# Performance work log

Measured on AMD Instinct MI355X. Metric: run time of the kernel, lower is better.

## Reference

```python
import jax, jax.numpy as jnp
import numpy as np

NUM_USERS = 50000
NUM_ITEMS = 50000
N_NODES = NUM_USERS + NUM_ITEMS
DIM_FEAT = 256
HID = 128
EMB = 128
K = 3
N_EDGES = 1_600_000


def setup_inputs() -> dict:
    key = jax.random.key(0)
    ks = jax.random.split(key, 16)

    def xavier(k, shape):
        fan_in, fan_out = shape[-2], shape[-1]
        std = float(np.sqrt(2.0 / (fan_in + fan_out)))
        return jax.random.normal(k, shape, dtype=jnp.float32) * std

    return {
        "feat": jax.random.normal(ks[0], (NUM_ITEMS, DIM_FEAT), dtype=jnp.float32),
        "node_emb": jax.random.normal(ks[1], (N_NODES, EMB), dtype=jnp.float32),
        "src": jax.random.randint(ks[2], (N_EDGES,), 0, N_NODES, dtype=jnp.int32),
        "dst": jax.random.randint(ks[3], (N_EDGES,), 0, N_NODES, dtype=jnp.int32),
        "user_feat_emb": xavier(ks[4], (NUM_USERS, HID)),
        "trans_w": xavier(ks[5], (DIM_FEAT, HID)),
        "trans_b": jnp.zeros((HID,), dtype=jnp.float32),
        # layer 0: hidden->hidden; layers 1,2: emb->emb. hidden==emb so stack.
        "ws": xavier(ks[6], (K, HID, HID)),
        "des_w": xavier(ks[7], (K, HID, EMB)),
        "des_b": jnp.zeros((K, EMB), dtype=jnp.float32),
        # concat=True: outs[i] takes [h | u] of width hidden+emb
        "out_w": xavier(ks[8], (K, HID + EMB, EMB)),
        "out_b": jnp.zeros((K, EMB), dtype=jnp.float32),
    }


def reference(feat, node_emb, src, dst, user_feat_emb,
              trans_w, trans_b, ws, des_w, des_b, out_w, out_b):
    # feat = trans(feat); concat user embeddings; L2-normalize rows
    x = feat @ trans_w + trans_b                      # [num_items, HID]
    x = jnp.concatenate([user_feat_emb, x], axis=0)   # [N, HID]
    norm = jnp.linalg.norm(x, axis=1, keepdims=True)
    x = x / jnp.maximum(norm, 1e-12)

    lrelu = jax.nn.leaky_relu  # slope 0.01, matches F.leaky_relu default
    for i in range(K):
        # g.func(x, W): sparse adjacency aggregation (sum over in-edges) then dense W
        agg = jax.ops.segment_sum(x[src], dst, num_segments=N_NODES)  # [N, HID]
        h = lrelu(agg @ ws[i])                                        # [N, HID]
        u = lrelu(h @ des_w[i] + des_b[i] + node_emb)                 # [N, EMB]
        x = lrelu(jnp.concatenate([h, u], axis=1) @ out_w[i] + out_b[i])
    return x, user_feat_emb
```

## Files before the change

kernel.cpp:

```cpp
#include <hip/hip_runtime.h>

#define NN 100000
#define NU 50000
#define NI 50000
#define NE 1600000
#define NSLICE 3
#define SLICEW 33334

#define HSLICE 4
#define HCHUNK 64
#define HSW 25600
#define HEPC (NE/HCHUNK)

typedef unsigned short u16;
typedef unsigned int u32;

typedef __attribute__((ext_vector_type(8))) short s16x8;
typedef __attribute__((ext_vector_type(4))) float f32x4;
typedef __attribute__((ext_vector_type(4))) unsigned short us4;

__device__ __forceinline__ float bf2f(u16 u){
  union { u32 i; float f; } v; v.i = ((u32)u) << 16; return v.f;
}
__device__ __forceinline__ u16 f2bf(float f){
  union { float f; u32 i; } v; v.f = f;
  u32 u = v.i;
  return (u16)((u + 0x7FFFu + ((u >> 16) & 1u)) >> 16);
}
__device__ __forceinline__ u32 pack2(float lo, float hi){
  return (u32)f2bf(lo) | ((u32)f2bf(hi) << 16);
}
__device__ __forceinline__ float lrelu(float x){ return x > 0.f ? x : 0.01f * x; }
__device__ __forceinline__ float san(float v){
  union { float f; u32 i; } u; u.f = v;
  return ((u.i & 0x7F800000u) == 0x7F800000u) ? 0.f : v;
}

__global__ __launch_bounds__(256) void transpose_weights(
    const float* __restrict__ trans_w, const float* __restrict__ wsw,
    const float* __restrict__ desw, const float* __restrict__ outw,
    u16* __restrict__ Ttw, u16* __restrict__ Tw, u16* __restrict__ Td, u16* __restrict__ To)
{
  __shared__ u16 L[128][136];
  int b = blockIdx.x, t = threadIdx.x;
  const float* src; u16* dst; int stride;
  if (b < 2)      { src = trans_w + b*16384;        dst = Ttw + b*128;          stride = 256; }
  else if (b < 5) { int i = b-2; src = wsw  + i*16384; dst = Tw + i*16384;      stride = 128; }
  else if (b < 8) { int i = b-5; src = desw + i*16384; dst = Td + i*16384;      stride = 128; }
  else            { int i = (b-8)>>1, h = (b-8)&1;
                    src = outw + i*32768 + h*16384;    dst = To + i*32768 + h*128; stride = 256; }
  #pragma unroll
  for (int p = 0; p < 8; p++){
    int fi = (p*256 + t)*8;
    int r = fi >> 7, c = fi & 127;
    f32x4 v0 = *(const f32x4*)(src + r*128 + c);
    f32x4 v1 = *(const f32x4*)(src + r*128 + c + 4);
    L[c+0][r] = f2bf(san(v0.x)); L[c+1][r] = f2bf(san(v0.y));
    L[c+2][r] = f2bf(san(v0.z)); L[c+3][r] = f2bf(san(v0.w));
    L[c+4][r] = f2bf(san(v1.x)); L[c+5][r] = f2bf(san(v1.y));
    L[c+6][r] = f2bf(san(v1.z)); L[c+7][r] = f2bf(san(v1.w));
  }
  __syncthreads();
  #pragma unroll
  for (int p = 0; p < 8; p++){
    int fi = (p*256 + t)*8;
    int n = fi >> 7, k = fi & 127;
    us4 o0, o1;
    o0.x = L[n][k+0]; o0.y = L[n][k+1]; o0.z = L[n][k+2]; o0.w = L[n][k+3];
    o1.x = L[n][k+4]; o1.y = L[n][k+5]; o1.z = L[n][k+6]; o1.w = L[n][k+7];
    *(us4*)(dst + (size_t)n*stride + k)     = o0;
    *(us4*)(dst + (size_t)n*stride + k + 4) = o1;
  }
}

__global__ __launch_bounds__(256) void conv_nemb(
    const float* __restrict__ nemb, u16* __restrict__ nembB)
{
  int i = blockIdx.x*256 + threadIdx.x;
  size_t off = (size_t)i * 8;
  f32x4 v0 = *(const f32x4*)(nemb + off);
  f32x4 v1 = *(const f32x4*)(nemb + off + 4);
  us4 o0, o1;
  o0.x = f2bf(san(v0.x)); o0.y = f2bf(san(v0.y)); o0.z = f2bf(san(v0.z)); o0.w = f2bf(san(v0.w));
  o1.x = f2bf(san(v1.x)); o1.y = f2bf(san(v1.y)); o1.z = f2bf(san(v1.z)); o1.w = f2bf(san(v1.w));
  *(us4*)(nembB + off)     = o0;
  *(us4*)(nembB + off + 4) = o1;
}

__global__ __launch_bounds__(256) void norm_users(const float* __restrict__ ufe, u16* __restrict__ X)
{
  int gid = blockIdx.x*256 + threadIdx.x;
  int row = gid >> 6, lane = gid & 63;
  float2 v = *(const float2*)(ufe + (size_t)row*128 + lane*2);
  float a = san(v.x), b = san(v.y);
  float ss = a*a + b*b;
  #pragma unroll
  for (int off = 32; off; off >>= 1) ss += __shfl_xor(ss, off, 64);
  float inv = 1.0f / fmaxf(sqrtf(ss), 1e-12f);
  *(u32*)(X + (size_t)row*128 + lane*2) = pack2(a*inv, b*inv);
}

__global__ __launch_bounds__(256, 4) void trans_items(
    const float* __restrict__ feat, const u16* __restrict__ Ttw,
    const float* __restrict__ tb, u16* __restrict__ X)
{
  __shared__ u16 Af[64][136];
  __shared__ float rowss[64][8];
  __shared__ float rnorm[64];

  int t = threadIdx.x;
  int r0 = blockIdx.x * 64;
  int w = t >> 6, lane = t & 63;
  int l15 = lane & 15, q = lane >> 4;
  int m0 = (w & 1) * 64, n0 = (w >> 1) * 32;

  f32x4 acc[4][2];
  #pragma unroll
  for (int mi = 0; mi < 4; mi++)
    #pragma unroll
    for (int ni = 0; ni < 2; ni++){ acc[mi][ni].x = 0.f; acc[mi][ni].y = 0.f; acc[mi][ni].z = 0.f; acc[mi][ni].w = 0.f; }

  for (int half = 0; half < 2; half++){
    __syncthreads();
    #pragma unroll
    for (int p = 0; p < 4; p++){
      int fi = (p*256 + t)*8;
      int r = fi >> 7, c = fi & 127;
      int row = r0 + r;
      us4 o0 = {0,0,0,0}, o1 = {0,0,0,0};
      if (row < NI){
        f32x4 v0 = *(const f32x4*)(feat + (size_t)row*256 + half*128 + c);
        f32x4 v1 = *(const f32x4*)(feat + (size_t)row*256 + half*128 + c + 4);
        o0.x = f2bf(san(v0.x)); o0.y = f2bf(san(v0.y)); o0.z = f2bf(san(v0.z)); o0.w = f2bf(san(v0.w));
        o1.x = f2bf(san(v1.x)); o1.y = f2bf(san(v1.y)); o1.z = f2bf(san(v1.z)); o1.w = f2bf(san(v1.w));
      }
      *(us4*)&Af[r][c]     = o0;
      *(us4*)&Af[r][c + 4] = o1;
    }
    __syncthreads();
    #pragma unroll
    for (int kc = 0; kc < 128; kc += 32){
      s16x8 afr[4], bfr[2];
      #pragma unroll
      for (int mi = 0; mi < 4; mi++)
        afr[mi] = *(const s16x8*)(Ttw + (size_t)(m0 + 16*mi + l15)*256 + half*128 + kc + 8*q);
      #pragma unroll
      for (int ni = 0; ni < 2; ni++) bfr[ni] = *(const s16x8*)&Af[n0 + 16*ni + l15][kc + 8*q];
      #pragma unroll
      for (int mi = 0; mi < 4; mi++)
        #pragma unroll
        for (int ni = 0; ni < 2; ni++)
          acc[mi][ni] = __builtin_amdgcn_mfma_f32_16x16x32_bf16(afr[mi], bfr[ni], acc[mi][ni], 0, 0, 0);
    }
  }

  float bias[4][4];
  #pragma unroll
  for (int mi = 0; mi < 4; mi++){
    int c0 = m0 + 16*mi + 4*q;
    f32x4 bv = *(const f32x4*)(tb + c0);
    bias[mi][0] = san(bv.x); bias[mi][1] = san(bv.y); bias[mi][2] = san(bv.z); bias[mi][3] = san(bv.w);
  }
  #pragma unroll
  for (int ni = 0; ni < 2; ni++){
    float ss = 0.f;
    #pragma unroll
    for (int mi = 0; mi < 4; mi++){
      float v0 = acc[mi][ni].x + bias[mi][0];
      float v1 = acc[mi][ni].y + bias[mi][1];
      float v2 = acc[mi][ni].z + bias[mi][2];
      float v3 = acc[mi][ni].w + bias[mi][3];
      ss += v0*v0 + v1*v1 + v2*v2 + v3*v3;
    }
    rowss[n0 + 16*ni + l15][(w & 1)*4 + q] = ss;
  }
  __syncthreads();
  if (t < 64){
    float s = 0.f;
    #pragma unroll
    for (int j = 0; j < 8; j++) s += rowss[t][j];
    rnorm[t] = 1.0f / fmaxf(sqrtf(s), 1e-12f);
  }
  __syncthreads();
  #pragma unroll
  for (int mi = 0; mi < 4; mi++){
    int c0 = m0 + 16*mi + 4*q;
    #pragma unroll
    for (int ni = 0; ni < 2; ni++){
      int r = n0 + 16*ni + l15;
      int row = r0 + r;
      if (row < NI){
        float inv = rnorm[r];
        us4 o;
        o.x = f2bf((acc[mi][ni].x + bias[mi][0]) * inv);
        o.y = f2bf((acc[mi][ni].y + bias[mi][1]) * inv);
        o.z = f2bf((acc[mi][ni].z + bias[mi][2]) * inv);
        o.w = f2bf((acc[mi][ni].w + bias[mi][3]) * inv);
        *(us4*)(X + (size_t)(NU + row)*128 + c0) = o;
      }
    }
  }
}

__global__ __launch_bounds__(1024) void hist_lds(
    const int* __restrict__ dst, u32* __restrict__ countsC)
{
  __shared__ u32 cnt[HSW];
  int b = blockIdx.x;
  int s = b / HCHUNK, c = b % HCHUNK;
  int t = threadIdx.x;
  for (int i = t; i < HSW; i += 1024) cnt[i] = 0;
  __syncthreads();
  int lo = s * HSW;
  int hi = min(lo + HSW, NN);
  int e0 = c * HEPC, e1 = e0 + HEPC;
  for (int e = e0 + t*4; e < e1; e += 4096){
    int4 d4 = *(const int4*)(dst + e);
    int d0 = min(max(d4.x, 0), NN-1);
    int d1 = min(max(d4.y, 0), NN-1);
    int d2 = min(max(d4.z, 0), NN-1);
    int d3 = min(max(d4.w, 0), NN-1);
    if (d0 >= lo && d0 < hi) atomicAdd(&cnt[d0 - lo], 1u);
    if (d1 >= lo && d1 < hi) atomicAdd(&cnt[d1 - lo], 1u);
    if (d2 >= lo && d2 < hi) atomicAdd(&cnt[d2 - lo], 1u);
    if (d3 >= lo && d3 < hi) atomicAdd(&cnt[d3 - lo], 1u);
  }
  __syncthreads();
  u32* outp = countsC + (size_t)c*NN + lo;
  int w = hi - lo;
  for (int i = t; i < w; i += 1024) outp[i] = cnt[i];
}

__global__ __launch_bounds__(256) void reduce_counts(
    const u32* __restrict__ countsC, int* __restrict__ counts)
{
  int v = blockIdx.x*256 + threadIdx.x;
  if (v < NN){
    u32 sum = 0;
    #pragma unroll
    for (int c = 0; c < HCHUNK; c++) sum += countsC[(size_t)c*NN + v];
    counts[v] = (int)sum;
  }
}

__global__ __launch_bounds__(1024) void scan_k(const int* __restrict__ counts, int* __restrict__ row_ptr){
  __shared__ int wsum[16];
  __shared__ int woff[16];
  __shared__ int tot;
  int t = threadIdx.x;
  int lane = t & 63, wid = t >> 6;
  int carry = 0;
  for (int base = 0; base < NN; base += 4096){
    int idx = base + t*4;
    int4 v = {0,0,0,0};
    if (idx < NN) v = *(const int4*)(counts + idx);
    int s4 = v.x + v.y + v.z + v.w;
    int s = s4;
    #pragma unroll
    for (int off = 1; off < 64; off <<= 1){
      int u = __shfl_up(s, off, 64);
      if (lane >= off) s += u;
    }
    if (lane == 63) wsum[wid] = s;
    __syncthreads();
    if (t < 16){
      int ws = wsum[t];
      int wscan = ws;
      #pragma unroll
      for (int off = 1; off < 16; off <<= 1){
        int u = __shfl_up(wscan, off, 64);
        if (t >= off) wscan += u;
      }
      woff[t] = wscan - ws;
      if (t == 15) tot = wscan;
    }
    __syncthreads();
    if (idx < NN){
      int e0 = carry + woff[wid] + (s - s4);
      int4 o;
      o.x = e0; o.y = e0 + v.x; o.z = o.y + v.y; o.w = o.z + v.z;
      *(int4*)(row_ptr + idx) = o;
    }
    carry += tot;
    __syncthreads();
  }
}

__global__ __launch_bounds__(256) void fill_slice(
    const int* __restrict__ src, const int* __restrict__ dst,
    int* __restrict__ row_ptr, int* __restrict__ esrc, int d0, int d1)
{
  int e = blockIdx.x*256 + threadIdx.x;
  if (e < NE){
    int d = dst[e];
    if (d >= d0 && d < d1){
      d = min(max(d, 0), NN - 1);
      int pos = atomicAdd(&row_ptr[d], 1);
      pos = min(max(pos, 0), NE - 1);
      esrc[pos] = src[e];
    }
  }
}

#define ACC8(P) \
  a0 += bf2f((u16)(P.x & 0xFFFF)); a1 += bf2f((u16)(P.x >> 16)); \
  a2 += bf2f((u16)(P.y & 0xFFFF)); a3 += bf2f((u16)(P.y >> 16)); \
  a4 += bf2f((u16)(P.z & 0xFFFF)); a5 += bf2f((u16)(P.z >> 16)); \
  a6 += bf2f((u16)(P.w & 0xFFFF)); a7 += bf2f((u16)(P.w >> 16));

__global__ __launch_bounds__(256) void aggregate(
    const u16* __restrict__ X, const int* __restrict__ row_ptr,
    const int* __restrict__ esrc, u16* __restrict__ AGG)
{
  int gid = blockIdx.x*256 + threadIdx.x;
  int v = gid >> 6, lane = gid & 63;
  int sub = lane >> 4, li = lane & 15;
  int jb = (v == 0) ? 0 : row_ptr[v - 1];
  int je = row_ptr[v];
  jb = min(max(jb, 0), NE);
  je = min(max(je, jb), NE);

  float a0=0.f,a1=0.f,a2=0.f,a3=0.f,a4=0.f,a5=0.f,a6=0.f,a7=0.f;

  int j = jb + sub;
  for (; j + 12 < je; j += 16){
    int s0 = esrc[j];      s0 = min(max(s0, 0), NN - 1);
    int s1 = esrc[j + 4];  s1 = min(max(s1, 0), NN - 1);
    int s2 = esrc[j + 8];  s2 = min(max(s2, 0), NN - 1);
    int s3 = esrc[j + 12]; s3 = min(max(s3, 0), NN - 1);
    uint4 p0 = *(const uint4*)(X + (size_t)s0*128 + li*8);
    uint4 p1 = *(const uint4*)(X + (size_t)s1*128 + li*8);
    uint4 p2 = *(const uint4*)(X + (size_t)s2*128 + li*8);
    uint4 p3 = *(const uint4*)(X + (size_t)s3*128 + li*8);
    ACC8(p0); ACC8(p1); ACC8(p2); ACC8(p3);
  }
  for (; j + 4 < je; j += 8){
    int s0 = esrc[j];     s0 = min(max(s0, 0), NN - 1);
    int s1 = esrc[j + 4]; s1 = min(max(s1, 0), NN - 1);
    uint4 p0 = *(const uint4*)(X + (size_t)s0*128 + li*8);
    uint4 p1 = *(const uint4*)(X + (size_t)s1*128 + li*8);
    ACC8(p0); ACC8(p1);
  }
  for (; j < je; j += 4){
    int s0 = esrc[j]; s0 = min(max(s0, 0), NN - 1);
    uint4 p0 = *(const uint4*)(X + (size_t)s0*128 + li*8);
    ACC8(p0);
  }

  a0 += __shfl_xor(a0, 16, 64); a0 += __shfl_xor(a0, 32, 64);
  a1 += __shfl_xor(a1, 16, 64); a1 += __shfl_xor(a1, 32, 64);
  a2 += __shfl_xor(a2, 16, 64); a2 += __shfl_xor(a2, 32, 64);
  a3 += __shfl_xor(a3, 16, 64); a3 += __shfl_xor(a3, 32, 64);
  a4 += __shfl_xor(a4, 16, 64); a4 += __shfl_xor(a4, 32, 64);
  a5 += __shfl_xor(a5, 16, 64); a5 += __shfl_xor(a5, 32, 64);
  a6 += __shfl_xor(a6, 16, 64); a6 += __shfl_xor(a6, 32, 64);
  a7 += __shfl_xor(a7, 16, 64); a7 += __shfl_xor(a7, 32, 64);

  if (sub == 0){
    uint4 o;
    o.x = pack2(a0, a1); o.y = pack2(a2, a3);
    o.z = pack2(a4, a5); o.w = pack2(a6, a7);
    *(uint4*)(AGG + (size_t)v*128 + li*8) = o;
  }
}

__global__ __launch_bounds__(256, 2) void layer_fused(
    const u16* __restrict__ AGG, const u16* __restrict__ nembB,
    const u16* __restrict__ Twi, const u16* __restrict__ Tdi,
    const float* __restrict__ dbF, const u16* __restrict__ Toi,
    const float* __restrict__ obF, u16* __restrict__ XoutB,
    float* __restrict__ XoutF, int last)
{
  __shared__ __align__(16) u16 Ab[128][136];
  __shared__ __align__(16) u16 Hb[128][136];

  int t = threadIdx.x;
  int r0 = blockIdx.x * 128;
  int w = t >> 6, lane = t & 63;
  int l15 = lane & 15, q = lane >> 4;
  int m0 = (w & 1) * 64, n0 = (w >> 1) * 64;

  f32x4 acc[4][4];

#define ZERO_ACC() \
  { _Pragma("unroll") for (int mi = 0; mi < 4; mi++) \
      { _Pragma("unroll") for (int ni = 0; ni < 4; ni++) \
        { acc[mi][ni].x = 0.f; acc[mi][ni].y = 0.f; acc[mi][ni].z = 0.f; acc[mi][ni].w = 0.f; } } }

#define GEMMG(BARR, WBASE, WSTRIDE, WKOFF) \
  { s16x8 afr[4][4]; \
    _Pragma("unroll") for (int mi = 0; mi < 4; mi++) \
      { _Pragma("unroll") for (int kk = 0; kk < 4; kk++) \
          afr[mi][kk] = *(const s16x8*)((WBASE) + (size_t)(m0 + 16*mi + l15)*(WSTRIDE) + (WKOFF) + kk*32 + 8*q); } \
    _Pragma("unroll") for (int kk = 0; kk < 4; kk++){ \
      s16x8 bfr[4]; \
      _Pragma("unroll") for (int ni = 0; ni < 4; ni++) bfr[ni] = *(const s16x8*)&BARR[n0 + 16*ni + l15][kk*32 + 8*q]; \
      _Pragma("unroll") for (int mi = 0; mi < 4; mi++) \
        { _Pragma("unroll") for (int ni = 0; ni < 4; ni++) \
          acc[mi][ni] = __builtin_amdgcn_mfma_f32_16x16x32_bf16(afr[mi][kk], bfr[ni], acc[mi][ni], 0, 0, 0); } } }

  #pragma unroll
  for (int p = 0; p < 8; p++){
    int fi = (p*256 + t)*8;
    int r = fi >> 7, c = fi & 127;
    int row = r0 + r;
    us4 o0 = {0,0,0,0}, o1 = {0,0,0,0};
    if (row < NN){
      o0 = *(const us4*)(AGG + (size_t)row*128 + c);
      o1 = *(const us4*)(AGG + (size_t)row*128 + c + 4);
    }
    *(us4*)&Ab[r][c]     = o0;
    *(us4*)&Ab[r][c + 4] = o1;
  }
  __syncthreads();

  ZERO_ACC();
  GEMMG(Ab, Twi, 128, 0);

  #pragma unroll
  for (int mi = 0; mi < 4; mi++){
    #pragma unroll
    for (int ni = 0; ni < 4; ni++){
      us4 o;
      o.x = f2bf(lrelu(acc[mi][ni].x));
      o.y = f2bf(lrelu(acc[mi][ni].y));
      o.z = f2bf(lrelu(acc[mi][ni].z));
      o.w = f2bf(lrelu(acc[mi][ni].w));
      *(us4*)&Hb[n0 + 16*ni + l15][m0 + 16*mi + 4*q] = o;
    }
  }
  __syncthreads();

  ZERO_ACC();
  GEMMG(Hb, Tdi, 128, 0);

  #pragma unroll
  for (int mi = 0; mi < 4; mi++){
    int c0 = m0 + 16*mi + 4*q;
    f32x4 dbv = *(const f32x4*)(dbF + c0);
    float db0 = san(dbv.x), db1 = san(dbv.y), db2 = san(dbv.z), db3 = san(dbv.w);
    #pragma unroll
    for (int ni = 0; ni < 4; ni++){
      int r = n0 + 16*ni + l15;
      int row = r0 + r;
      float e0 = 0.f, e1 = 0.f, e2 = 0.f, e3 = 0.f;
      if (row < NN){
        us4 ne = *(const us4*)(nembB + (size_t)row*128 + c0);
        e0 = bf2f(ne.x); e1 = bf2f(ne.y); e2 = bf2f(ne.z); e3 = bf2f(ne.w);
      }
      us4 o;
      o.x = f2bf(lrelu(acc[mi][ni].x + db0 + e0));
      o.y = f2bf(lrelu(acc[mi][ni].y + db1 + e1));
      o.z = f2bf(lrelu(acc[mi][ni].z + db2 + e2));
      o.w = f2bf(lrelu(acc[mi][ni].w + db3 + e3));
      *(us4*)&Ab[r][c0] = o;
    }
  }
  __syncthreads();

  ZERO_ACC();
  GEMMG(Hb, Toi, 256, 0);
  GEMMG(Ab, Toi, 256, 128);

  #pragma unroll
  for (int mi = 0; mi < 4; mi++){
    int c0 = m0 + 16*mi + 4*q;
    f32x4 obv = *(const f32x4*)(obF + c0);
    float b0 = san(obv.x), b1 = san(obv.y), b2 = san(obv.z), b3 = san(obv.w);
    #pragma unroll
    for (int ni = 0; ni < 4; ni++){
      int r = n0 + 16*ni + l15;
      int row = r0 + r;
      if (row < NN){
        if (last){
          f32x4 o;
          o.x = lrelu(acc[mi][ni].x + b0);
          o.y = lrelu(acc[mi][ni].y + b1);
          o.z = lrelu(acc[mi][ni].z + b2);
          o.w = lrelu(acc[mi][ni].w + b3);
          *(f32x4*)(XoutF + (size_t)row*128 + c0) = o;
        } else {
          us4 o;
          o.x = f2bf(lrelu(acc[mi][ni].x + b0));
          o.y = f2bf(lrelu(acc[mi][ni].y + b1));
          o.z = f2bf(lrelu(acc[mi][ni].z + b2));
          o.w = f2bf(lrelu(acc[mi][ni].w + b3));
          *(us4*)(XoutB + (size_t)row*128 + c0) = o;
        }
      }
    }
  }
#undef ZERO_ACC
#undef GEMMG
}

__global__ void copy_ufe(const float4* __restrict__ s, float4* __restrict__ d, int n){
  int i = blockIdx.x*256 + threadIdx.x;
  if (i < n){
    float4 v = s[i];
    v.x = san(v.x); v.y = san(v.y); v.z = san(v.z); v.w = san(v.w);
    d[i] = v;
  }
}

extern "C" void kernel_launch(void* const* d_in, const int* in_sizes, int n_in,
                              void* d_out, int out_size, void* d_ws, size_t ws_size,
                              hipStream_t stream)
{
  const float* feat = (const float*)d_in[0];
  const float* nemb = (const float*)d_in[1];
  const int*   src  = (const int*)d_in[2];
  const int*   dst  = (const int*)d_in[3];
  const float* ufe  = (const float*)d_in[4];
  const float* tw   = (const float*)d_in[5];
  const float* tb   = (const float*)d_in[6];
  const float* wsw  = (const float*)d_in[7];
  const float* desw = (const float*)d_in[8];
  const float* desb = (const float*)d_in[9];
  const float* outw = (const float*)d_in[10];
  const float* outb = (const float*)d_in[11];

  float* out  = (float*)d_out;
  float* outU = out + (size_t)NN*128;

  u16* X = (u16*)out;
  u16* nembB = (u16*)outU;

  char* p = (char*)d_ws;
  u16*   AGG = (u16*)p;    p += (size_t)NN*128*2;
  u16*   Ttw = (u16*)p;    p += (size_t)2*16384*2;
  u16*   Tw  = (u16*)p;    p += (size_t)3*16384*2;
  u16*   Td  = (u16*)p;    p += (size_t)3*16384*2;
  u16*   To  = (u16*)p;    p += (size_t)3*32768*2;
  int* row_ptr = (int*)p;  p += (size_t)100004*4;
  int* counts  = (int*)p;  p += (size_t)100000*4;
  int* esrc    = (int*)p;  p += (size_t)NE*4;
  u32* countsC = (u32*)AGG;

  transpose_weights<<<14, 256, 0, stream>>>(tw, wsw, desw, outw, Ttw, Tw, Td, To);
  conv_nemb<<<6250, 256, 0, stream>>>(nemb, nembB);
  norm_users<<<NU/4, 256, 0, stream>>>(ufe, X);
  trans_items<<<(NI + 63)/64, 256, 0, stream>>>(feat, Ttw, tb, X);

  hist_lds<<<HSLICE*HCHUNK, 1024, 0, stream>>>(dst, countsC);
  reduce_counts<<<(NN + 255)/256, 256, 0, stream>>>(countsC, counts);
  scan_k<<<1, 1024, 0, stream>>>(counts, row_ptr);
  for (int s = 0; s < NSLICE; s++){
    fill_slice<<<(NE + 255)/256, 256, 0, stream>>>(src, dst, row_ptr, esrc,
        s*SLICEW, (s == NSLICE-1) ? NN : (s+1)*SLICEW);
  }

  for (int i = 0; i < 3; i++){
    aggregate<<<NN/4, 256, 0, stream>>>(X, row_ptr, esrc, AGG);
    layer_fused<<<(NN + 127)/128, 256, 0, stream>>>(AGG, nembB,
        Tw + (size_t)i*16384, Td + (size_t)i*16384, desb + (size_t)i*128,
        To + (size_t)i*32768, outb + (size_t)i*128, X, out, (i == 2) ? 1 : 0);
  }
  copy_ufe<<<(NU*128/4 + 255)/256, 256, 0, stream>>>((const float4*)ufe, (float4*)outU, NU*128/4);
}
```

Measured before the change: 710.4 us.

## Merge prep kernels, parallelize prefix scan across blocks, use fewer fill slices

Three preprocessing kernels (weight transpose, node-embedding conversion, user normalization) are merged into one launch selected by block index. The single-block serial prefix scan over 100k counts becomes a three-phase multi-block scan using block sums. The fill pass is cut from three dst slices to two, so the edge arrays are read fewer times, but each slice now has more atomic targets and weaker locality. Together these aim to cut launch overhead and the serial scan latency.

```diff
diff --git a/kernel.cpp b/kernel.cpp
--- a/kernel.cpp
+++ b/kernel.cpp
@@ -4,14 +4,18 @@
 #define NU 50000
 #define NI 50000
 #define NE 1600000
-#define NSLICE 3
-#define SLICEW 33334
+#define NSLICE 2
+#define SLICEW 50000
 
 #define HSLICE 4
 #define HCHUNK 64
 #define HSW 25600
 #define HEPC (NE/HCHUNK)
 
+#define PREP_TW 14
+#define PREP_CONV 6250
+#define PREP_NORM 12500
+
 typedef unsigned short u16;
 typedef unsigned int u32;
 
@@ -36,68 +40,66 @@
   return ((u.i & 0x7F800000u) == 0x7F800000u) ? 0.f : v;
 }
 
-__global__ __launch_bounds__(256) void transpose_weights(
+__global__ __launch_bounds__(256) void prep(
     const float* __restrict__ trans_w, const float* __restrict__ wsw,
     const float* __restrict__ desw, const float* __restrict__ outw,
-    u16* __restrict__ Ttw, u16* __restrict__ Tw, u16* __restrict__ Td, u16* __restrict__ To)
+    u16* __restrict__ Ttw, u16* __restrict__ Tw, u16* __restrict__ Td, u16* __restrict__ To,
+    const float* __restrict__ nemb, u16* __restrict__ nembB,
+    const float* __restrict__ ufe, u16* __restrict__ X)
 {
   __shared__ u16 L[128][136];
   int b = blockIdx.x, t = threadIdx.x;
-  const float* src; u16* dst; int stride;
-  if (b < 2)      { src = trans_w + b*16384;        dst = Ttw + b*128;          stride = 256; }
-  else if (b < 5) { int i = b-2; src = wsw  + i*16384; dst = Tw + i*16384;      stride = 128; }
-  else if (b < 8) { int i = b-5; src = desw + i*16384; dst = Td + i*16384;      stride = 128; }
-  else            { int i = (b-8)>>1, h = (b-8)&1;
-                    src = outw + i*32768 + h*16384;    dst = To + i*32768 + h*128; stride = 256; }
-  #pragma unroll
-  for (int p = 0; p < 8; p++){
-    int fi = (p*256 + t)*8;
-    int r = fi >> 7, c = fi & 127;
-    f32x4 v0 = *(const f32x4*)(src + r*128 + c);
-    f32x4 v1 = *(const f32x4*)(src + r*128 + c + 4);
-    L[c+0][r] = f2bf(san(v0.x)); L[c+1][r] = f2bf(san(v0.y));
-    L[c+2][r] = f2bf(san(v0.z)); L[c+3][r] = f2bf(san(v0.w));
-    L[c+4][r] = f2bf(san(v1.x)); L[c+5][r] = f2bf(san(v1.y));
-    L[c+6][r] = f2bf(san(v1.z)); L[c+7][r] = f2bf(san(v1.w));
-  }
-  __syncthreads();
-  #pragma unroll
-  for (int p = 0; p < 8; p++){
-    int fi = (p*256 + t)*8;
-    int n = fi >> 7, k = fi & 127;
+
+  if (b < PREP_TW){
+    const float* src; u16* dst; int stride;
+    if (b < 2)      { src = trans_w + b*16384;        dst = Ttw + b*128;          stride = 256; }
+    else if (b < 5) { int i = b-2; src = wsw  + i*16384; dst = Tw + i*16384;      stride = 128; }
+    else if (b < 8) { int i = b-5; src = desw + i*16384; dst = Td + i*16384;      stride = 128; }
+    else            { int i = (b-8)>>1, h = (b-8)&1;
+                      src = outw + i*32768 + h*16384;    dst = To + i*32768 + h*128; stride = 256; }
+    #pragma unroll
+    for (int p = 0; p < 8; p++){
+      int fi = (p*256 + t)*8;
+      int r = fi >> 7, c = fi & 127;
+      f32x4 v0 = *(const f32x4*)(src + r*128 + c);
+      f32x4 v1 = *(const f32x4*)(src + r*128 + c + 4);
+      L[c+0][r] = f2bf(san(v0.x)); L[c+1][r] = f2bf(san(v0.y));
+      L[c+2][r] = f2bf(san(v0.z)); L[c+3][r] = f2bf(san(v0.w));
+      L[c+4][r] = f2bf(san(v1.x)); L[c+5][r] = f2bf(san(v1.y));
+      L[c+6][r] = f2bf(san(v1.z)); L[c+7][r] = f2bf(san(v1.w));
+    }
+    __syncthreads();
+    #pragma unroll
+    for (int p = 0; p < 8; p++){
+      int fi = (p*256 + t)*8;
+      int n = fi >> 7, k = fi & 127;
+      us4 o0, o1;
+      o0.x = L[n][k+0]; o0.y = L[n][k+1]; o0.z = L[n][k+2]; o0.w = L[n][k+3];
+      o1.x = L[n][k+4]; o1.y = L[n][k+5]; o1.z = L[n][k+6]; o1.w = L[n][k+7];
+      *(us4*)(dst + (size_t)n*stride + k)     = o0;
+      *(us4*)(dst + (size_t)n*stride + k + 4) = o1;
+    }
+  } else if (b < PREP_TW + PREP_CONV){
+    int i = (b - PREP_TW)*256 + t;
+    size_t off = (size_t)i * 8;
+    f32x4 v0 = *(const f32x4*)(nemb + off);
+    f32x4 v1 = *(const f32x4*)(nemb + off + 4);
     us4 o0, o1;
-    o0.x = L[n][k+0]; o0.y = L[n][k+1]; o0.z = L[n][k+2]; o0.w = L[n][k+3];
-    o1.x = L[n][k+4]; o1.y = L[n][k+5]; o1.z = L[n][k+6]; o1.w = L[n][k+7];
-    *(us4*)(dst + (size_t)n*stride + k)     = o0;
-    *(us4*)(dst + (size_t)n*stride + k + 4) = o1;
-  }
-}
-
-__global__ __launch_bounds__(256) void conv_nemb(
-    const float* __restrict__ nemb, u16* __restrict__ nembB)
-{
-  int i = blockIdx.x*256 + threadIdx.x;
-  size_t off = (size_t)i * 8;
-  f32x4 v0 = *(const f32x4*)(nemb + off);
-  f32x4 v1 = *(const f32x4*)(nemb + off + 4);
-  us4 o0, o1;
-  o0.x = f2bf(san(v0.x)); o0.y = f2bf(san(v0.y)); o0.z = f2bf(san(v0.z)); o0.w = f2bf(san(v0.w));
-  o1.x = f2bf(san(v1.x)); o1.y = f2bf(san(v1.y)); o1.z = f2bf(san(v1.z)); o1.w = f2bf(san(v1.w));
-  *(us4*)(nembB + off)     = o0;
-  *(us4*)(nembB + off + 4) = o1;
-}
-
-__global__ __launch_bounds__(256) void norm_users(const float* __restrict__ ufe, u16* __restrict__ X)
-{
-  int gid = blockIdx.x*256 + threadIdx.x;
-  int row = gid >> 6, lane = gid & 63;
-  float2 v = *(const float2*)(ufe + (size_t)row*128 + lane*2);
-  float a = san(v.x), b = san(v.y);
-  float ss = a*a + b*b;
-  #pragma unroll
-  for (int off = 32; off; off >>= 1) ss += __shfl_xor(ss, off, 64);
-  float inv = 1.0f / fmaxf(sqrtf(ss), 1e-12f);
-  *(u32*)(X + (size_t)row*128 + lane*2) = pack2(a*inv, b*inv);
+    o0.x = f2bf(san(v0.x)); o0.y = f2bf(san(v0.y)); o0.z = f2bf(san(v0.z)); o0.w = f2bf(san(v0.w));
+    o1.x = f2bf(san(v1.x)); o1.y = f2bf(san(v1.y)); o1.z = f2bf(san(v1.z)); o1.w = f2bf(san(v1.w));
+    *(us4*)(nembB + off)     = o0;
+    *(us4*)(nembB + off + 4) = o1;
+  } else {
+    int gid = (b - PREP_TW - PREP_CONV)*256 + t;
+    int row = gid >> 6, lane = gid & 63;
+    float2 v = *(const float2*)(ufe + (size_t)row*128 + lane*2);
+    float a = san(v.x), bb = san(v.y);
+    float ss = a*a + bb*bb;
+    #pragma unroll
+    for (int off = 32; off; off >>= 1) ss += __shfl_xor(ss, off, 64);
+    float inv = 1.0f / fmaxf(sqrtf(ss), 1e-12f);
+    *(u32*)(X + (size_t)row*128 + lane*2) = pack2(a*inv, bb*inv);
+  }
 }
 
 __global__ __launch_bounds__(256, 4) void trans_items(
@@ -243,46 +245,68 @@
   }
 }
 
-__global__ __launch_bounds__(1024) void scan_k(const int* __restrict__ counts, int* __restrict__ row_ptr){
+__global__ __launch_bounds__(1024) void scan_p1(
+    const int* __restrict__ counts, int* __restrict__ row_ptr, int* __restrict__ bsum)
+{
   __shared__ int wsum[16];
   __shared__ int woff[16];
-  __shared__ int tot;
   int t = threadIdx.x;
   int lane = t & 63, wid = t >> 6;
-  int carry = 0;
-  for (int base = 0; base < NN; base += 4096){
-    int idx = base + t*4;
-    int4 v = {0,0,0,0};
-    if (idx < NN) v = *(const int4*)(counts + idx);
-    int s4 = v.x + v.y + v.z + v.w;
-    int s = s4;
-    #pragma unroll
-    for (int off = 1; off < 64; off <<= 1){
-      int u = __shfl_up(s, off, 64);
-      if (lane >= off) s += u;
-    }
-    if (lane == 63) wsum[wid] = s;
-    __syncthreads();
-    if (t < 16){
-      int ws = wsum[t];
-      int wscan = ws;
-      #pragma unroll
-      for (int off = 1; off < 16; off <<= 1){
-        int u = __shfl_up(wscan, off, 64);
-        if (t >= off) wscan += u;
-      }
-      woff[t] = wscan - ws;
-      if (t == 15) tot = wscan;
-    }
-    __syncthreads();
-    if (idx < NN){
-      int e0 = carry + woff[wid] + (s - s4);
-      int4 o;
-      o.x = e0; o.y = e0 + v.x; o.z = o.y + v.y; o.w = o.z + v.z;
-      *(int4*)(row_ptr + idx) = o;
-    }
-    carry += tot;
-    __syncthreads();
+  int idx = blockIdx.x*4096 + t*4;
+  int4 v = {0,0,0,0};
+  if (idx < NN) v = *(const int4*)(counts + idx);
+  int s4 = v.x + v.y + v.z + v.w;
+  int s = s4;
+  #pragma unroll
+  for (int off = 1; off < 64; off <<= 1){
+    int u = __shfl_up(s, off, 64);
+    if (lane >= off) s += u;
+  }
+  if (lane == 63) wsum[wid] = s;
+  __syncthreads();
+  if (t < 16){
+    int ws = wsum[t];
+    int wscan = ws;
+    #pragma unroll
+    for (int off = 1; off < 16; off <<= 1){
+      int u = __shfl_up(wscan, off, 64);
+      if (t >= off) wscan += u;
+    }
+    woff[t] = wscan - ws;
+    if (t == 15) bsum[blockIdx.x] = wscan;
+  }
+  __syncthreads();
+  if (idx < NN){
+    int e0 = woff[wid] + (s - s4);
+    int4 o;
+    o.x = e0; o.y = e0 + v.x; o.z = o.y + v.y; o.w = o.z + v.z;
+    *(int4*)(row_ptr + idx) = o;
+  }
+}
+
+__global__ __launch_bounds__(64) void scan_p2(int* __restrict__ bsum, int nb)
+{
+  int t = threadIdx.x;
+  int v = (t < nb) ? bsum[t] : 0;
+  int s = v;
+  #pragma unroll
+  for (int off = 1; off < 64; off <<= 1){
+    int u = __shfl_up(s, off, 64);
+    if (t >= off) s += u;
+  }
+  if (t < nb) bsum[t] = s - v;
+}
+
+__global__ __launch_bounds__(1024) void scan_p3(
+    int* __restrict__ row_ptr, const int* __restrict__ bsum)
+{
+  int c = bsum[blockIdx.x];
+  if (c == 0) return;
+  int idx = blockIdx.x*4096 + threadIdx.x*4;
+  if (idx < NN){
+    int4 o = *(int4*)(row_ptr + idx);
+    o.x += c; o.y += c; o.z += c; o.w += c;
+    *(int4*)(row_ptr + idx) = o;
   }
 }
 
@@ -534,17 +558,20 @@
   u16*   To  = (u16*)p;    p += (size_t)3*32768*2;
   int* row_ptr = (int*)p;  p += (size_t)100004*4;
   int* counts  = (int*)p;  p += (size_t)100000*4;
+  int* bsum    = (int*)p;  p += (size_t)64*4;
   int* esrc    = (int*)p;  p += (size_t)NE*4;
   u32* countsC = (u32*)AGG;
 
-  transpose_weights<<<14, 256, 0, stream>>>(tw, wsw, desw, outw, Ttw, Tw, Td, To);
-  conv_nemb<<<6250, 256, 0, stream>>>(nemb, nembB);
-  norm_users<<<NU/4, 256, 0, stream>>>(ufe, X);
+  prep<<<PREP_TW + PREP_CONV + PREP_NORM, 256, 0, stream>>>(
+      tw, wsw, desw, outw, Ttw, Tw, Td, To, nemb, nembB, ufe, X);
   trans_items<<<(NI + 63)/64, 256, 0, stream>>>(feat, Ttw, tb, X);
 
   hist_lds<<<HSLICE*HCHUNK, 1024, 0, stream>>>(dst, countsC);
   reduce_counts<<<(NN + 255)/256, 256, 0, stream>>>(countsC, counts);
-  scan_k<<<1, 1024, 0, stream>>>(counts, row_ptr);
+  int nsb = (NN + 4095)/4096;
+  scan_p1<<<nsb, 1024, 0, stream>>>(counts, row_ptr, bsum);
+  scan_p2<<<1, 64, 0, stream>>>(bsum, nsb);
+  scan_p3<<<nsb, 1024, 0, stream>>>(row_ptr, bsum);
   for (int s = 0; s < NSLICE; s++){
     fill_slice<<<(NE + 255)/256, 256, 0, stream>>>(src, dst, row_ptr, esrc,
         s*SLICEW, (s == NSLICE-1) ? NN : (s+1)*SLICEW);
```

After: 693.2 us. 1.02x faster.
